# Kernel optimization log

Measured on AMD Instinct MI355X. Metric: run time of the kernel, lower is better.

Reference implementation:

```python
import jax, jax.numpy as jnp
import numpy as np

B, S, D, H = 2, 2048, 1024, 16
HD = D // H  # head_dim = 64


def setup_inputs() -> dict:
    key = jax.random.key(0)
    ks = jax.random.split(key, 5)
    scale = 0.02
    x = jax.random.normal(ks[0], (B, S, D), dtype=jnp.float32)
    Wq = scale * jax.random.normal(ks[1], (H, D, HD), dtype=jnp.float32)
    Wk = scale * jax.random.normal(ks[2], (H, D, HD), dtype=jnp.float32)
    Wv = scale * jax.random.normal(ks[3], (H, D, HD), dtype=jnp.float32)
    Wo = scale * jax.random.normal(ks[4], (D, D), dtype=jnp.float32)
    bq = jnp.zeros((H, HD), dtype=jnp.float32)
    bk = jnp.zeros((H, HD), dtype=jnp.float32)
    bv = jnp.zeros((H, HD), dtype=jnp.float32)
    bo = jnp.zeros((D,), dtype=jnp.float32)
    return {"x": x, "Wq": Wq, "bq": bq, "Wk": Wk, "bk": bk,
            "Wv": Wv, "bv": bv, "Wo": Wo, "bo": bo}


def reference(x, Wq, bq, Wk, bk, Wv, bv, Wo, bo):
    # Per-head QKV projections (the torch module's per-head nn.Linear list,
    # vectorized over the head axis h). Dropout is identity (eval mode).
    q = jnp.einsum("bsd,hde->bhse", x, Wq) + bq[None, :, None, :]  # [B,H,S,HD]
    k = jnp.einsum("bsd,hde->bhse", x, Wk) + bk[None, :, None, :]
    v = jnp.einsum("bsd,hde->bhse", x, Wv) + bv[None, :, None, :]

    norm = jnp.asarray(np.sqrt(HD), dtype=x.dtype)
    scores = jnp.einsum("bhse,bhte->bhst", q, k) / norm  # [B,H,S,S]
    causal = jnp.tril(jnp.ones((S, S), dtype=bool))
    scores = jnp.where(causal[None, None], scores, jnp.asarray(-jnp.inf, dtype=scores.dtype))
    attn = jax.nn.softmax(scores, axis=-1)

    wv = jnp.einsum("bhst,bhte->bhse", attn, v)          # [B,H,S,HD]
    wv = jnp.transpose(wv, (0, 2, 1, 3)).reshape(B, S, D)  # concat heads on last dim
    out = wv @ Wo.T + bo                                   # output projection
    return out
```

## Files before the change

### kernel.cpp

```cpp
#include <hip/hip_runtime.h>


#define DD 1024
#define SS 2048
#define BB 2
#define HH 16
#define HD 64
#define QSCALE 0.18033688011112042f
#define LSTR 88

typedef __attribute__((ext_vector_type(8))) short short8;
typedef __attribute__((ext_vector_type(4))) float float4v;
typedef unsigned short ushort;
typedef unsigned int uint;

__device__ inline ushort f2bf(float f) {
    union { float f; uint i; } v; v.f = f;
    uint r = v.i + 0x7FFF + ((v.i >> 16) & 1);
    return (ushort)(r >> 16);
}
__device__ inline ushort f2bf_f(float f) {
    union { float f; uint i; } v; v.f = f;
    return (ushort)((v.i + 0x8000u) >> 16);
}

__device__ __forceinline__ void cp16(const ushort* g, ushort* l) {
    __builtin_amdgcn_global_load_lds((const __attribute__((address_space(1))) void*)g,
                                     (__attribute__((address_space(3))) void*)l,
                                     16, 0, 0);
}

__global__ __launch_bounds__(256) void cvt_all(const float* __restrict__ x,
                                               const float* __restrict__ Wo,
                                               ushort* __restrict__ xb,
                                               ushort* __restrict__ Wob) {
    const int NX4 = (BB * SS * DD) / 4;
    int i = blockIdx.x * 256 + threadIdx.x;
    const float* src; ushort* dst; int j;
    if (i < NX4) { src = x; dst = xb; j = i; }
    else         { src = Wo; dst = Wob; j = i - NX4; }
    float4 v = ((const float4*)src)[j];
    ushort o[4] = { f2bf(v.x), f2bf(v.y), f2bf(v.z), f2bf(v.w) };
    ((uint2*)dst)[j] = *(const uint2*)o;
}

__global__ __launch_bounds__(256) void transpose_w3(const float* __restrict__ Wq,
                                                    const float* __restrict__ Wk,
                                                    const float* __restrict__ Wv,
                                                    ushort* __restrict__ W3T) {
    __shared__ ushort T[64][65];
    int z = blockIdx.z;
    const float* W = z == 0 ? Wq : (z == 1 ? Wk : Wv);
    int h = blockIdx.y, d0 = blockIdx.x * 64;
    const float* Wh = W + h * DD * HD;
    ushort* Wt = W3T + ((size_t)z * HH + h) * HD * DD;
    int t = threadIdx.x;
    #pragma unroll
    for (int i = 0; i < 4; i++) {
        int idx = t + i * 256;
        int d = idx >> 4, e4 = (idx & 15) * 4;
        float4 v = *(const float4*)(Wh + (d0 + d) * HD + e4);
        T[d][e4 + 0] = f2bf(v.x); T[d][e4 + 1] = f2bf(v.y);
        T[d][e4 + 2] = f2bf(v.z); T[d][e4 + 3] = f2bf(v.w);
    }
    __syncthreads();
    #pragma unroll
    for (int i = 0; i < 2; i++) {
        int idx = t + i * 256;
        int e = idx >> 3, d8 = (idx & 7) * 8;
        ushort tmp[8];
        #pragma unroll
        for (int j = 0; j < 8; j++) tmp[j] = T[d8 + j][e];
        *(uint4*)(Wt + e * DD + d0 + d8) = *(uint4*)tmp;
    }
}

__global__ __launch_bounds__(256) void gemm_qkv(const ushort* __restrict__ xb,
                                                const ushort* __restrict__ W3T,
                                                const float* __restrict__ bq,
                                                const float* __restrict__ bk,
                                                const float* __restrict__ bv,
                                                ushort* __restrict__ qb,
                                                ushort* __restrict__ kb,
                                                ushort* __restrict__ vT) {
    __shared__ ushort Al[128 * 32];
    __shared__ ushort Bl[128 * 32];
    int z = blockIdx.z;
    const ushort* Wt   = W3T + (size_t)z * HH * HD * DD;
    const float*  bias = z == 0 ? bq : (z == 1 ? bk : bv);
    int m0 = blockIdx.x * 128, n0 = blockIdx.y * 128;
    int t = threadIdx.x, lane = t & 63, w = t >> 6;
    int wm = w & 1, wn = w >> 1;
    int qm = lane >> 4, lm = lane & 15;

    float4v acc[4][4] = {};
    for (int k0 = 0; k0 < DD; k0 += 32) {
        __syncthreads();
        #pragma unroll
        for (int r2 = 0; r2 < 2; r2++) {
            int c = t + r2 * 256;
            cp16(xb + (size_t)(m0 + (c >> 2)) * DD + k0 + (c & 3) * 8, Al + c * 8);
            cp16(Wt + (size_t)(n0 + (c >> 2)) * DD + k0 + (c & 3) * 8, Bl + c * 8);
        }
        __syncthreads();
        short8 a[4], b[4];
        #pragma unroll
        for (int i = 0; i < 4; i++)
            a[i] = *(const short8*)(Al + (wm * 64 + i * 16 + lm) * 32 + qm * 8);
        #pragma unroll
        for (int j = 0; j < 4; j++)
            b[j] = *(const short8*)(Bl + (wn * 64 + j * 16 + lm) * 32 + qm * 8);
        if (z == 2) {
            #pragma unroll
            for (int i = 0; i < 4; i++)
                #pragma unroll
                for (int j = 0; j < 4; j++)
                    acc[i][j] = __builtin_amdgcn_mfma_f32_16x16x32_bf16(a[i], b[j], acc[i][j], 0, 0, 0);
        } else {
            #pragma unroll
            for (int i = 0; i < 4; i++)
                #pragma unroll
                for (int j = 0; j < 4; j++)
                    acc[i][j] = __builtin_amdgcn_mfma_f32_16x16x32_bf16(b[j], a[i], acc[i][j], 0, 0, 0);
        }
    }
    if (z == 2) {
        #pragma unroll
        for (int j = 0; j < 4; j++) {
            int n = n0 + wn * 64 + j * 16 + lm;
            int h = n >> 6, e = n & 63;
            float bb = bias[n];
            #pragma unroll
            for (int i = 0; i < 4; i++) {
                int m = m0 + wm * 64 + i * 16 + qm * 4;
                int b_ = m >> 11, s = m & (SS - 1);
                ushort p4[4];
                #pragma unroll
                for (int r = 0; r < 4; r++) p4[r] = f2bf_f(acc[i][j][r] + bb);
                *(uint2*)(vT + ((size_t)(b_ * HH + h) * HD + e) * SS + s) = *(const uint2*)p4;
            }
        }
    } else {
        ushort* Out = z == 0 ? qb : kb;
        float sc = z == 0 ? QSCALE : 1.0f;
        #pragma unroll
        for (int j = 0; j < 4; j++) {
            int nb = n0 + wn * 64 + j * 16 + qm * 4;
            float4 b4 = *(const float4*)(bias + nb);
            #pragma unroll
            for (int i = 0; i < 4; i++) {
                int m = m0 + wm * 64 + i * 16 + lm;
                ushort p4[4];
                p4[0] = f2bf_f((acc[i][j][0] + b4.x) * sc);
                p4[1] = f2bf_f((acc[i][j][1] + b4.y) * sc);
                p4[2] = f2bf_f((acc[i][j][2] + b4.z) * sc);
                p4[3] = f2bf_f((acc[i][j][3] + b4.w) * sc);
                *(uint2*)(Out + (size_t)m * DD + nb) = *(const uint2*)p4;
            }
        }
    }
}

__global__ __launch_bounds__(512, 4) void attn(const ushort* __restrict__ Q,
                                               const ushort* __restrict__ K,
                                               const ushort* __restrict__ VT,
                                               ushort* __restrict__ O) {
    __shared__ ushort QP[128][LSTR];
    __shared__ ushort Kl[2][64][LSTR];
    __shared__ ushort Vl[2][64][LSTR];
    int bh = blockIdx.x, px = blockIdx.y;
    int qt = 15 - px;
    int b = bh >> 4, h = bh & 15;
    int m0 = qt * 128;
    int njt = 2 * (qt + 1);
    const ushort* Qp = Q + (size_t)b * SS * DD + h * HD;
    const ushort* Kp = K + (size_t)b * SS * DD + h * HD;
    const ushort* Vp = VT + (size_t)bh * HD * SS;
    int t = threadIdx.x, lane = t & 63, w = t >> 6;
    int qm = lane >> 4, lm = lane & 15;
    int row0 = t >> 3, colc = (t & 7) * 8;

    *(uint4*)(&QP[row0][colc])      = *(const uint4*)(Qp + (size_t)(m0 + row0) * DD + colc);
    *(uint4*)(&QP[row0 + 64][colc]) = *(const uint4*)(Qp + (size_t)(m0 + row0 + 64) * DD + colc);
    *(uint4*)(&Kl[0][row0][colc])   = *(const uint4*)(Kp + (size_t)row0 * DD + colc);
    *(uint4*)(&Vl[0][row0][colc])   = *(const uint4*)(Vp + (size_t)row0 * SS + colc);
    __syncthreads();

    short8 qf[2];
    qf[0] = *(const short8*)(&QP[w * 16 + lm][qm * 8]);
    qf[1] = *(const short8*)(&QP[w * 16 + lm][32 + qm * 8]);

    float4v o[4] = {};
    float mi = -__builtin_inff(), li = 0.f;
    int cur = 0;
    int qg = m0 + w * 16 + lm;

    for (int jt = 0; jt < njt; jt++) {
        if (jt) __syncthreads();
        bool pre = jt + 1 < njt;
        uint4 pk, pv;
        if (pre) {
            int nn = (jt + 1) * 64;
            pk = *(const uint4*)(Kp + (size_t)(nn + row0) * DD + colc);
            pv = *(const uint4*)(Vp + (size_t)row0 * SS + nn + colc);
        }

        float4v s[4] = {};
        #pragma unroll
        for (int kc = 0; kc < 2; kc++) {
            #pragma unroll
            for (int j = 0; j < 4; j++) {
                short8 ak = *(const short8*)(&Kl[cur][j * 16 + lm][kc * 32 + qm * 8]);
                s[j] = __builtin_amdgcn_mfma_f32_16x16x32_bf16(ak, qf[kc], s[j], 0, 0, 0);
            }
        }
        if (jt >= 2 * qt) {
            #pragma unroll
            for (int j = 0; j < 4; j++)
                #pragma unroll
                for (int r = 0; r < 4; r++)
                    if (jt * 64 + j * 16 + qm * 4 + r > qg) s[j][r] = -__builtin_inff();
        }
        float mloc = s[0][0];
        #pragma unroll
        for (int j = 0; j < 4; j++)
            #pragma unroll
            for (int r = 0; r < 4; r++) mloc = fmaxf(mloc, s[j][r]);
        mloc = fmaxf(mloc, __shfl_xor(mloc, 16, 64));
        mloc = fmaxf(mloc, __shfl_xor(mloc, 32, 64));
        float mnew = fmaxf(mi, mloc);
        float sum = 0.f;
        #pragma unroll
        for (int j = 0; j < 4; j++)
            #pragma unroll
            for (int r = 0; r < 4; r++) {
                float p = __builtin_amdgcn_exp2f(s[j][r] - mnew);
                s[j][r] = p;
                sum += p;
            }
        sum += __shfl_xor(sum, 16, 64);
        sum += __shfl_xor(sum, 32, 64);
        float alpha = __builtin_amdgcn_exp2f(mi - mnew);
        li = li * alpha + sum;
        mi = mnew;

        #pragma unroll
        for (int j = 0; j < 4; j++) {
            ushort p4[4];
            #pragma unroll
            for (int r = 0; r < 4; r++) p4[r] = f2bf_f(s[j][r]);
            *(uint2*)(&QP[w * 16 + lm][j * 16 + qm * 4]) = *(const uint2*)p4;
        }
        #pragma unroll
        for (int jn = 0; jn < 4; jn++)
            #pragma unroll
            for (int r = 0; r < 4; r++) o[jn][r] *= alpha;
        asm volatile("s_waitcnt lgkmcnt(0)" ::: "memory");

        #pragma unroll
        for (int kc = 0; kc < 2; kc++) {
            short8 ap = *(const short8*)(&QP[w * 16 + lm][kc * 32 + qm * 8]);
            #pragma unroll
            for (int jn = 0; jn < 4; jn++) {
                short8 av = *(const short8*)(&Vl[cur][jn * 16 + lm][kc * 32 + qm * 8]);
                o[jn] = __builtin_amdgcn_mfma_f32_16x16x32_bf16(av, ap, o[jn], 0, 0, 0);
            }
        }
        if (pre) {
            *(uint4*)(&Kl[cur ^ 1][row0][colc]) = pk;
            *(uint4*)(&Vl[cur ^ 1][row0][colc]) = pv;
        }
        cur ^= 1;
    }
    float inv = 1.f / li;
    ushort* Ob = O + ((size_t)b * SS + qg) * DD + h * HD;
    #pragma unroll
    for (int jn = 0; jn < 4; jn++) {
        ushort p4[4];
        #pragma unroll
        for (int r = 0; r < 4; r++) p4[r] = f2bf_f(o[jn][r] * inv);
        *(uint2*)(Ob + jn * 16 + qm * 4) = *(const uint2*)p4;
    }
}

__global__ __launch_bounds__(256) void gemm_out(const ushort* __restrict__ X,
                                                const ushort* __restrict__ Wob,
                                                const float* __restrict__ bo,
                                                float* __restrict__ Out) {
    __shared__ ushort Al[128 * 32];
    __shared__ ushort Bl[64 * 32];
    int m0 = blockIdx.x * 128, n0 = blockIdx.y * 64;
    int t = threadIdx.x, lane = t & 63, w = t >> 6;
    int wm = w & 1, wn = w >> 1;
    int qm = lane >> 4, lm = lane & 15;

    float4v acc[4][2] = {};
    for (int k0 = 0; k0 < DD; k0 += 32) {
        __syncthreads();
        #pragma unroll
        for (int r2 = 0; r2 < 2; r2++) {
            int c = t + r2 * 256;
            cp16(X + (size_t)(m0 + (c >> 2)) * DD + k0 + (c & 3) * 8, Al + c * 8);
        }
        cp16(Wob + (size_t)(n0 + (t >> 2)) * DD + k0 + (t & 3) * 8, Bl + t * 8);
        __syncthreads();
        short8 a[4], b[2];
        #pragma unroll
        for (int i = 0; i < 4; i++)
            a[i] = *(const short8*)(Al + (wm * 64 + i * 16 + lm) * 32 + qm * 8);
        #pragma unroll
        for (int j = 0; j < 2; j++)
            b[j] = *(const short8*)(Bl + (wn * 32 + j * 16 + lm) * 32 + qm * 8);
        #pragma unroll
        for (int i = 0; i < 4; i++)
            #pragma unroll
            for (int j = 0; j < 2; j++)
                acc[i][j] = __builtin_amdgcn_mfma_f32_16x16x32_bf16(b[j], a[i], acc[i][j], 0, 0, 0);
    }
    #pragma unroll
    for (int j = 0; j < 2; j++) {
        int nb = n0 + wn * 32 + j * 16 + qm * 4;
        float4 b4 = *(const float4*)(bo + nb);
        #pragma unroll
        for (int i = 0; i < 4; i++) {
            int m = m0 + wm * 64 + i * 16 + lm;
            float4 st;
            st.x = acc[i][j][0] + b4.x;
            st.y = acc[i][j][1] + b4.y;
            st.z = acc[i][j][2] + b4.z;
            st.w = acc[i][j][3] + b4.w;
            *(float4*)(Out + (size_t)m * DD + nb) = st;
        }
    }
}

extern "C" void kernel_launch(void* const* d_in, const int* in_sizes, int n_in,
                              void* d_out, int out_size, void* d_ws, size_t ws_size,
                              hipStream_t stream) {
    const float* x   = (const float*)d_in[0];
    const float* Wq  = (const float*)d_in[1];
    const float* bq  = (const float*)d_in[2];
    const float* Wk  = (const float*)d_in[3];
    const float* bk  = (const float*)d_in[4];
    const float* Wv_ = (const float*)d_in[5];
    const float* bv  = (const float*)d_in[6];
    const float* Wo  = (const float*)d_in[7];
    const float* bo  = (const float*)d_in[8];
    float* out = (float*)d_out;

    ushort* xb  = (ushort*)d_ws;
    ushort* W3T = xb  + (size_t)BB * SS * DD;
    ushort* Wob = W3T + (size_t)3 * HH * HD * DD;
    ushort* qb  = Wob + (size_t)DD * DD;
    ushort* kb  = qb + (size_t)BB * SS * DD;
    ushort* vT  = kb + (size_t)BB * SS * DD;
    ushort* wvb = vT + (size_t)BB * SS * DD;

    cvt_all<<<dim3(5120), 256, 0, stream>>>(x, Wo, xb, Wob);
    transpose_w3<<<dim3(16, 16, 3), 256, 0, stream>>>(Wq, Wk, Wv_, W3T);
    gemm_qkv<<<dim3(32, 8, 3), 256, 0, stream>>>(xb, W3T, bq, bk, bv, qb, kb, vT);
    attn<<<dim3(32, 16), 512, 0, stream>>>(qb, kb, vT, wvb);
    gemm_out<<<dim3(32, 16), 256, 0, stream>>>(wvb, Wob, bo, out);
}
```

Measured before the change: 205.6 us.

## Double GEMM K-tile to 64 with XOR-swizzled LDS and merge prep kernels

The QKV and output GEMMs now stage a 64-wide K slice per iteration instead of 32, which halves the number of barrier-separated load phases. LDS rows are XOR-swizzled in 16-byte chunks so that MFMA fragment reads avoid bank conflicts. The conversion and weight-transpose kernels are merged into a single prep launch to save one kernel launch. The cost is twice the LDS per block, which may lower occupancy.

```diff
diff --git a/kernel.cpp b/kernel.cpp
--- a/kernel.cpp
+++ b/kernel.cpp
@@ -30,34 +30,33 @@
                                      16, 0, 0);
 }
 
-__global__ __launch_bounds__(256) void cvt_all(const float* __restrict__ x,
-                                               const float* __restrict__ Wo,
-                                               ushort* __restrict__ xb,
-                                               ushort* __restrict__ Wob) {
-    const int NX4 = (BB * SS * DD) / 4;
-    int i = blockIdx.x * 256 + threadIdx.x;
-    const float* src; ushort* dst; int j;
-    if (i < NX4) { src = x; dst = xb; j = i; }
-    else         { src = Wo; dst = Wob; j = i - NX4; }
-    float4 v = ((const float4*)src)[j];
-    ushort o[4] = { f2bf(v.x), f2bf(v.y), f2bf(v.z), f2bf(v.w) };
-    ((uint2*)dst)[j] = *(const uint2*)o;
-}
-
-__global__ __launch_bounds__(256) void transpose_w3(const float* __restrict__ Wq,
-                                                    const float* __restrict__ Wk,
-                                                    const float* __restrict__ Wv,
-                                                    ushort* __restrict__ W3T) {
+__global__ __launch_bounds__(256) void prep(const float* __restrict__ x,
+                                            const float* __restrict__ Wo,
+                                            const float* __restrict__ Wq,
+                                            const float* __restrict__ Wk,
+                                            const float* __restrict__ Wv,
+                                            ushort* __restrict__ xb,
+                                            ushort* __restrict__ Wob,
+                                            ushort* __restrict__ W3T) {
     __shared__ ushort T[64][65];
-    int z = blockIdx.z;
+    int bid = blockIdx.x, t = threadIdx.x;
+    if (bid < 5120) {
+        const float* src; ushort* dst; int j;
+        if (bid < 4096) { src = x;  dst = xb;  j = bid * 256 + t; }
+        else            { src = Wo; dst = Wob; j = (bid - 4096) * 256 + t; }
+        float4 v = ((const float4*)src)[j];
+        ushort o[4] = { f2bf(v.x), f2bf(v.y), f2bf(v.z), f2bf(v.w) };
+        ((uint2*)dst)[j] = *(const uint2*)o;
+        return;
+    }
+    int i = bid - 5120;
+    int z = i >> 8, h = (i >> 4) & 15, d0 = (i & 15) * 64;
     const float* W = z == 0 ? Wq : (z == 1 ? Wk : Wv);
-    int h = blockIdx.y, d0 = blockIdx.x * 64;
     const float* Wh = W + h * DD * HD;
     ushort* Wt = W3T + ((size_t)z * HH + h) * HD * DD;
-    int t = threadIdx.x;
     #pragma unroll
-    for (int i = 0; i < 4; i++) {
-        int idx = t + i * 256;
+    for (int s = 0; s < 4; s++) {
+        int idx = t + s * 256;
         int d = idx >> 4, e4 = (idx & 15) * 4;
         float4 v = *(const float4*)(Wh + (d0 + d) * HD + e4);
         T[d][e4 + 0] = f2bf(v.x); T[d][e4 + 1] = f2bf(v.y);
@@ -65,8 +64,8 @@
     }
     __syncthreads();
     #pragma unroll
-    for (int i = 0; i < 2; i++) {
-        int idx = t + i * 256;
+    for (int s = 0; s < 2; s++) {
+        int idx = t + s * 256;
         int e = idx >> 3, d8 = (idx & 7) * 8;
         ushort tmp[8];
         #pragma unroll
@@ -83,8 +82,8 @@
                                                 ushort* __restrict__ qb,
                                                 ushort* __restrict__ kb,
                                                 ushort* __restrict__ vT) {
-    __shared__ ushort Al[128 * 32];
-    __shared__ ushort Bl[128 * 32];
+    __shared__ ushort Al[128 * 64];
+    __shared__ ushort Bl[128 * 64];
     int z = blockIdx.z;
     const ushort* Wt   = W3T + (size_t)z * HH * HD * DD;
     const float*  bias = z == 0 ? bq : (z == 1 ? bk : bv);
@@ -94,34 +93,40 @@
     int qm = lane >> 4, lm = lane & 15;
 
     float4v acc[4][4] = {};
-    for (int k0 = 0; k0 < DD; k0 += 32) {
+    for (int k0 = 0; k0 < DD; k0 += 64) {
         __syncthreads();
         #pragma unroll
-        for (int r2 = 0; r2 < 2; r2++) {
-            int c = t + r2 * 256;
-            cp16(xb + (size_t)(m0 + (c >> 2)) * DD + k0 + (c & 3) * 8, Al + c * 8);
-            cp16(Wt + (size_t)(n0 + (c >> 2)) * DD + k0 + (c & 3) * 8, Bl + c * 8);
+        for (int s = 0; s < 4; s++) {
+            int c = t + s * 256;
+            int row = c >> 3;
+            int j = (c & 7) ^ (row & 7);
+            cp16(xb + (size_t)(m0 + row) * DD + k0 + j * 8, Al + c * 8);
+            cp16(Wt + (size_t)(n0 + row) * DD + k0 + j * 8, Bl + c * 8);
         }
         __syncthreads();
-        short8 a[4], b[4];
-        #pragma unroll
-        for (int i = 0; i < 4; i++)
-            a[i] = *(const short8*)(Al + (wm * 64 + i * 16 + lm) * 32 + qm * 8);
-        #pragma unroll
-        for (int j = 0; j < 4; j++)
-            b[j] = *(const short8*)(Bl + (wn * 64 + j * 16 + lm) * 32 + qm * 8);
-        if (z == 2) {
+        #pragma unroll
+        for (int h2 = 0; h2 < 2; h2++) {
+            int sw = ((((h2 << 2) | qm) ^ (lm & 7)) << 3);
+            short8 a[4], b[4];
             #pragma unroll
             for (int i = 0; i < 4; i++)
-                #pragma unroll
-                for (int j = 0; j < 4; j++)
-                    acc[i][j] = __builtin_amdgcn_mfma_f32_16x16x32_bf16(a[i], b[j], acc[i][j], 0, 0, 0);
-        } else {
-            #pragma unroll
-            for (int i = 0; i < 4; i++)
-                #pragma unroll
-                for (int j = 0; j < 4; j++)
-                    acc[i][j] = __builtin_amdgcn_mfma_f32_16x16x32_bf16(b[j], a[i], acc[i][j], 0, 0, 0);
+                a[i] = *(const short8*)(Al + ((wm * 64 + i * 16 + lm) << 6) + sw);
+            #pragma unroll
+            for (int j = 0; j < 4; j++)
+                b[j] = *(const short8*)(Bl + ((wn * 64 + j * 16 + lm) << 6) + sw);
+            if (z == 2) {
+                #pragma unroll
+                for (int i = 0; i < 4; i++)
+                    #pragma unroll
+                    for (int j = 0; j < 4; j++)
+                        acc[i][j] = __builtin_amdgcn_mfma_f32_16x16x32_bf16(a[i], b[j], acc[i][j], 0, 0, 0);
+            } else {
+                #pragma unroll
+                for (int i = 0; i < 4; i++)
+                    #pragma unroll
+                    for (int j = 0; j < 4; j++)
+                        acc[i][j] = __builtin_amdgcn_mfma_f32_16x16x32_bf16(b[j], a[i], acc[i][j], 0, 0, 0);
+            }
         }
     }
     if (z == 2) {
@@ -287,35 +292,47 @@
                                                 const ushort* __restrict__ Wob,
                                                 const float* __restrict__ bo,
                                                 float* __restrict__ Out) {
-    __shared__ ushort Al[128 * 32];
-    __shared__ ushort Bl[64 * 32];
+    __shared__ ushort Al[128 * 64];
+    __shared__ ushort Bl[64 * 64];
     int m0 = blockIdx.x * 128, n0 = blockIdx.y * 64;
     int t = threadIdx.x, lane = t & 63, w = t >> 6;
     int wm = w & 1, wn = w >> 1;
     int qm = lane >> 4, lm = lane & 15;
 
     float4v acc[4][2] = {};
-    for (int k0 = 0; k0 < DD; k0 += 32) {
+    for (int k0 = 0; k0 < DD; k0 += 64) {
         __syncthreads();
         #pragma unroll
-        for (int r2 = 0; r2 < 2; r2++) {
-            int c = t + r2 * 256;
-            cp16(X + (size_t)(m0 + (c >> 2)) * DD + k0 + (c & 3) * 8, Al + c * 8);
-        }
-        cp16(Wob + (size_t)(n0 + (t >> 2)) * DD + k0 + (t & 3) * 8, Bl + t * 8);
+        for (int s = 0; s < 4; s++) {
+            int c = t + s * 256;
+            int row = c >> 3;
+            int j = (c & 7) ^ (row & 7);
+            cp16(X + (size_t)(m0 + row) * DD + k0 + j * 8, Al + c * 8);
+        }
+        #pragma unroll
+        for (int s = 0; s < 2; s++) {
+            int c = t + s * 256;
+            int row = c >> 3;
+            int j = (c & 7) ^ (row & 7);
+            cp16(Wob + (size_t)(n0 + row) * DD + k0 + j * 8, Bl + c * 8);
+        }
         __syncthreads();
-        short8 a[4], b[2];
-        #pragma unroll
-        for (int i = 0; i < 4; i++)
-            a[i] = *(const short8*)(Al + (wm * 64 + i * 16 + lm) * 32 + qm * 8);
-        #pragma unroll
-        for (int j = 0; j < 2; j++)
-            b[j] = *(const short8*)(Bl + (wn * 32 + j * 16 + lm) * 32 + qm * 8);
-        #pragma unroll
-        for (int i = 0; i < 4; i++)
+        #pragma unroll
+        for (int h2 = 0; h2 < 2; h2++) {
+            int sw = ((((h2 << 2) | qm) ^ (lm & 7)) << 3);
+            short8 a[4], b[2];
+            #pragma unroll
+            for (int i = 0; i < 4; i++)
+                a[i] = *(const short8*)(Al + ((wm * 64 + i * 16 + lm) << 6) + sw);
             #pragma unroll
             for (int j = 0; j < 2; j++)
-                acc[i][j] = __builtin_amdgcn_mfma_f32_16x16x32_bf16(b[j], a[i], acc[i][j], 0, 0, 0);
+                b[j] = *(const short8*)(Bl + ((wn * 32 + j * 16 + lm) << 6) + sw);
+            #pragma unroll
+            for (int i = 0; i < 4; i++)
+                #pragma unroll
+                for (int j = 0; j < 2; j++)
+                    acc[i][j] = __builtin_amdgcn_mfma_f32_16x16x32_bf16(b[j], a[i], acc[i][j], 0, 0, 0);
+        }
     }
     #pragma unroll
     for (int j = 0; j < 2; j++) {
@@ -356,8 +373,7 @@
     ushort* vT  = kb + (size_t)BB * SS * DD;
     ushort* wvb = vT + (size_t)BB * SS * DD;
 
-    cvt_all<<<dim3(5120), 256, 0, stream>>>(x, Wo, xb, Wob);
-    transpose_w3<<<dim3(16, 16, 3), 256, 0, stream>>>(Wq, Wk, Wv_, W3T);
+    prep<<<dim3(5888), 256, 0, stream>>>(x, Wo, Wq, Wk, Wv_, xb, Wob, W3T);
     gemm_qkv<<<dim3(32, 8, 3), 256, 0, stream>>>(xb, W3T, bq, bk, bv, qb, kb, vT);
     attn<<<dim3(32, 16), 512, 0, stream>>>(qb, kb, vT, wvb);
     gemm_out<<<dim3(32, 16), 256, 0, stream>>>(wvb, Wob, bo, out);
```

Result: faster. 195.8 us (-4.8%).
